# Kernel tuning notes

Hardware: AMD Instinct MI355X
Metric: run time of the kernel (lower is better)

Reference implementation:

```python
import jax, jax.numpy as jnp
import numpy as np

B, S, D, MD = 4, 4096, 1024, 512
SCALE = 0.02  # init scale for weights


def _layernorm(x, g, b, eps=1e-5):
    m = jnp.mean(x, axis=-1, keepdims=True)
    v = jnp.mean((x - m) ** 2, axis=-1, keepdims=True)
    return (x - m) * jax.lax.rsqrt(v + eps) * g + b


def _mem_mlp(h, W0, W1):
    # MemoryMLP depth=2: linear -> gelu -> linear (no biases)
    return jax.nn.gelu(h @ W0) @ W1


def _assoc_scan(gates, inputs):
    # state_t = g_t * state_{t-1} + in_t, over the seq axis (axis=1)
    def step(state, gi):
        g, i = gi
        s = g * state + i
        return s, s
    init = jnp.zeros_like(inputs[:, 0])
    _, out = jax.lax.scan(step, init, (jnp.moveaxis(gates, 1, 0), jnp.moveaxis(inputs, 1, 0)))
    return jnp.moveaxis(out, 1, 0)


def setup_inputs() -> dict:
    key = jax.random.key(0)
    ks = jax.random.split(key, 10)
    return {
        "x": jax.random.normal(ks[0], (B, S, D), jnp.float32),
        "Wd": jax.random.normal(ks[1], (D, MD), jnp.float32) * SCALE,
        "bd": jnp.zeros((MD,), jnp.float32),
        "Wu": jax.random.normal(ks[2], (MD, D), jnp.float32) * SCALE,
        "bu": jnp.zeros((D,), jnp.float32),
        "Wq": jax.random.normal(ks[3], (MD, MD), jnp.float32) * SCALE,
        "bq": jnp.zeros((MD,), jnp.float32),
        "Wk": jax.random.normal(ks[4], (MD, MD), jnp.float32) * SCALE,
        "bk": jnp.zeros((MD,), jnp.float32),
        "Wv": jax.random.normal(ks[5], (MD, MD), jnp.float32) * SCALE,
        "bv": jnp.zeros((MD,), jnp.float32),
        "q_gamma": jnp.ones((MD,), jnp.float32),
        "q_beta": jnp.zeros((MD,), jnp.float32),
        "k_gamma": jnp.ones((MD,), jnp.float32),
        "k_beta": jnp.zeros((MD,), jnp.float32),
        "W0": jax.random.normal(ks[6], (MD, MD), jnp.float32) * SCALE,
        "W1": jax.random.normal(ks[7], (MD, MD), jnp.float32) * SCALE,
        "adaptive_lr": jnp.full((1,), 0.01, jnp.float32),
        "forget_factor": jnp.full((1,), 0.1, jnp.float32),
    }


def reference(x, Wd, bd, Wu, bu, Wq, bq, Wk, bk, Wv, bv,
              q_gamma, q_beta, k_gamma, k_beta, W0, W1,
              adaptive_lr, forget_factor):
    h = x @ Wd + bd                                   # [B,S,MD] down_proj
    q = _layernorm(h @ Wq + bq, q_gamma, q_beta)      # q_norm(to_queries)
    k = _layernorm(h @ Wk + bk, k_gamma, k_beta)      # k_norm(to_keys)
    v = h @ Wv + bv                                   # to_values
    retrieved = _mem_mlp(q, W0, W1)                   # memory read
    pred = _mem_mlp(k, W0, W1)                        # memory store pred
    # per-token surprise: MSE over feature dim
    surprise = jnp.mean((pred - v) ** 2, axis=-1, keepdims=True)  # [B,S,1]
    gate_val = 1.0 - jax.nn.sigmoid(forget_factor)[0]
    gates = jnp.full((B, S, 1), 1.0, jnp.float32) * gate_val
    inputs = adaptive_lr[0] * surprise * v            # surprise-weighted write
    scanned = _assoc_scan(gates, inputs)              # sequential recurrence
    out = (retrieved + scanned) @ Wu + bu             # up_proj
    return out
```

## Files before the change

kernel.cpp:

```cpp
#include <hip/hip_runtime.h>
#include <hip/hip_bf16.h>
#include <math.h>

#define B_    4
#define S_    4096
#define DD    1024
#define MD    512
#define NTOK  16384
#define CHUNK 32
#define NCH   128

typedef unsigned short u16;
typedef unsigned int u32;
typedef __attribute__((ext_vector_type(8))) short short8;
typedef __attribute__((ext_vector_type(4))) float f32x4;
typedef __attribute__((ext_vector_type(4))) unsigned short us4;

__device__ __forceinline__ float bf2f(u16 u) {
    u32 x = ((u32)u) << 16;
    return __builtin_bit_cast(float, x);
}
__device__ __forceinline__ u16 f2bf(float f) {
    u32 x = __builtin_bit_cast(u32, f);
    u32 lsb = (x >> 16) & 1u;
    x += 0x7fffu + lsb;
    return (u16)(x >> 16);
}
__device__ __forceinline__ float gelu_f(float x) {
    float x3 = x * x * x;
    return 0.5f * x * (1.0f + tanhf(0.7978845608028654f * (x + 0.044715f * x3)));
}
__device__ __forceinline__ float gate_from_ff(const float* ff) {
    return 1.0f - 1.0f / (1.0f + expf(-ff[0]));
}

#define GLDS(gp, lp) __builtin_amdgcn_global_load_lds( \
    (const __attribute__((address_space(1))) void*)(gp), \
    (__attribute__((address_space(3))) void*)(lp), 16, 0, 0)

template<int NF, int EPI, int HB, int OUTBF, int SEG>
__global__ __launch_bounds__(256) void gemm_bf16_k(
    const u16* __restrict__ A, const u16* __restrict__ BT,
    const float* __restrict__ bias0, const float* __restrict__ bias1,
    const float* __restrict__ bias2,
    void* __restrict__ out0, void* __restrict__ out1, void* __restrict__ out2,
    int N, int K, int M, int OM)
{
    constexpr int TN = 32 * NF;
    __shared__ __align__(16) u16 Al[2][128 * 32];
    __shared__ __align__(16) u16 Bl[2][TN * 32];
    const int tid = threadIdx.x;
    const int w = tid >> 6, l = tid & 63;
    const int rowBase = blockIdx.y * 128, colBase = blockIdx.x * TN;
    const int wm = (w >> 1) * 64, wn = (w & 1) * 16 * NF;

    const int srow = l >> 2;
    const int skoff = (l & 3) * 8;
    const u16* Ag0 = A + (size_t)(rowBase + w * 16 + srow) * K + skoff;
    const u16* Ag1 = A + (size_t)(rowBase + (w + 4) * 16 + srow) * K + skoff;
    const u16* Bg0 = BT + (size_t)(colBase + w * 16 + srow) * K + skoff;
    const u16* Bg1 = (NF == 4) ? BT + (size_t)(colBase + (w + 4) * 16 + srow) * K + skoff : nullptr;

    f32x4 acc[4][NF];
#pragma unroll
    for (int i = 0; i < 4; ++i)
#pragma unroll
        for (int j = 0; j < NF; ++j) acc[i][j] = (f32x4){0.f, 0.f, 0.f, 0.f};

    const int KT = K >> 5;
    GLDS(Ag0, &Al[0][(w * 16) * 32]);
    GLDS(Ag1, &Al[0][((w + 4) * 16) * 32]);
    GLDS(Bg0, &Bl[0][(w * 16) * 32]);
    if (NF == 4) GLDS(Bg1, &Bl[0][((w + 4) * 16) * 32]);
    __syncthreads();

    const int lr = l & 15;
    const int goff = (l >> 4) * 8;
    int cur = 0;
    for (int kt = 0; kt < KT; ++kt) {
        if (kt + 1 < KT) {
            const size_t ko = (size_t)(kt + 1) << 5;
            GLDS(Ag0 + ko, &Al[cur ^ 1][(w * 16) * 32]);
            GLDS(Ag1 + ko, &Al[cur ^ 1][((w + 4) * 16) * 32]);
            GLDS(Bg0 + ko, &Bl[cur ^ 1][(w * 16) * 32]);
            if (NF == 4) GLDS(Bg1 + ko, &Bl[cur ^ 1][((w + 4) * 16) * 32]);
        }
        short8 af[4], bfr[NF];
#pragma unroll
        for (int m = 0; m < 4; ++m)
            af[m] = *(const short8*)&Al[cur][(wm + m * 16 + lr) * 32 + goff];
#pragma unroll
        for (int n = 0; n < NF; ++n)
            bfr[n] = *(const short8*)&Bl[cur][(wn + n * 16 + lr) * 32 + goff];
#pragma unroll
        for (int m = 0; m < 4; ++m)
#pragma unroll
            for (int n = 0; n < NF; ++n)
                acc[m][n] = __builtin_amdgcn_mfma_f32_16x16x32_bf16(af[m], bfr[n], acc[m][n], 0, 0, 0);
        __syncthreads();
        cur ^= 1;
    }

    const int g4 = (l >> 4) * 4;
    const bool odd = l & 1;
#pragma unroll
    for (int n = 0; n < NF; ++n) {
        const int col = colBase + wn + n * 16 + lr;
        const int seg = SEG ? (col >> 9) : 0;
        const int lcol = SEG ? (col - (seg << 9)) : col;
        const float* bp = (seg == 0) ? bias0 : (seg == 1) ? bias1 : bias2;
        void* outp = (seg == 0) ? out0 : (seg == 1) ? out1 : out2;
        const float bj = HB ? bp[lcol] : 0.0f;
#pragma unroll
        for (int m = 0; m < 4; ++m) {
            const int row0 = rowBase + wm + m * 16 + g4;
            float vq[4];
#pragma unroll
            for (int q = 0; q < 4; ++q) {
                float vv = acc[m][n][q] + bj;
                if (EPI == 1) vv = gelu_f(vv);
                vq[q] = vv;
            }
            if (OUTBF) {
                float pv[4];
#pragma unroll
                for (int q = 0; q < 4; ++q) pv[q] = __shfl_xor(vq[q], 1);
                const int q0 = odd ? 2 : 0;
                u16* ob = (u16*)outp;
#pragma unroll
                for (int j = 0; j < 2; ++j) {
                    const int qq = q0 + j;
                    float lo = odd ? pv[qq] : vq[qq];
                    float hi = odd ? vq[qq] : pv[qq];
                    u32 word = (u32)f2bf(lo) | ((u32)f2bf(hi) << 16);
                    *(u32*)(ob + (size_t)(row0 + qq) * OM + (lcol & ~1)) = word;
                }
            } else {
#pragma unroll
                for (int q = 0; q < 4; ++q)
                    ((float*)outp)[(size_t)(row0 + q) * OM + lcol] = vq[q];
            }
        }
    }
}

__global__ __launch_bounds__(256) void cvt_bf16_k(const float* __restrict__ in,
                                                  u16* __restrict__ out, int n)
{
    size_t i = ((size_t)blockIdx.x * 256 + threadIdx.x) * 8;
    if (i + 8 > (size_t)n) return;
    float4 a = *(const float4*)(in + i);
    float4 b = *(const float4*)(in + i + 4);
    short8 o;
    o[0] = (short)f2bf(a.x); o[1] = (short)f2bf(a.y);
    o[2] = (short)f2bf(a.z); o[3] = (short)f2bf(a.w);
    o[4] = (short)f2bf(b.x); o[5] = (short)f2bf(b.y);
    o[6] = (short)f2bf(b.z); o[7] = (short)f2bf(b.w);
    *(short8*)(out + i) = o;
}

__global__ __launch_bounds__(256) void wtrans_k(const float* __restrict__ W,
                                                u16* __restrict__ WT, int K, int M)
{
    __shared__ float t[32][33];
    const int tx = threadIdx.x, ty = threadIdx.y;
    const int m0 = blockIdx.x * 32, k0 = blockIdx.y * 32;
#pragma unroll
    for (int i = 0; i < 4; ++i)
        t[ty + i * 8][tx] = W[(size_t)(k0 + ty + i * 8) * M + m0 + tx];
    __syncthreads();
#pragma unroll
    for (int i = 0; i < 4; ++i)
        WT[(size_t)(m0 + ty + i * 8) * K + k0 + tx] = f2bf(t[tx][ty + i * 8]);
}

__global__ __launch_bounds__(256) void wtrans5_k(
    const float* __restrict__ Wa, const float* __restrict__ Wb,
    const float* __restrict__ Wc, const float* __restrict__ Wd_,
    const float* __restrict__ We,
    u16* __restrict__ Ta, u16* __restrict__ Tb, u16* __restrict__ Tc,
    u16* __restrict__ Td, u16* __restrict__ Te)
{
    __shared__ float t[32][33];
    const float* W; u16* T;
    switch (blockIdx.z) {
        case 0: W = Wa; T = Ta; break;
        case 1: W = Wb; T = Tb; break;
        case 2: W = Wc; T = Tc; break;
        case 3: W = Wd_; T = Td; break;
        default: W = We; T = Te; break;
    }
    const int tx = threadIdx.x, ty = threadIdx.y;
    const int m0 = blockIdx.x * 32, k0 = blockIdx.y * 32;
#pragma unroll
    for (int i = 0; i < 4; ++i)
        t[ty + i * 8][tx] = W[(size_t)(k0 + ty + i * 8) * 512 + m0 + tx];
    __syncthreads();
#pragma unroll
    for (int i = 0; i < 4; ++i)
        T[(size_t)(m0 + ty + i * 8) * 512 + k0 + tx] = f2bf(t[tx][ty + i * 8]);
}

__global__ __launch_bounds__(256) void ln2_k(u16* __restrict__ X0, u16* __restrict__ X1,
                                             const float* __restrict__ g0, const float* __restrict__ b0,
                                             const float* __restrict__ g1, const float* __restrict__ b1)
{
    const int row = blockIdx.x, tid = threadIdx.x;
    u16* x = (blockIdx.y ? X1 : X0) + (size_t)row * MD;
    const float* g = blockIdx.y ? g1 : g0;
    const float* b = blockIdx.y ? b1 : b0;
    float v0 = bf2f(x[tid]), v1 = bf2f(x[tid + 256]);
    float s = v0 + v1, q = v0 * v0 + v1 * v1;
#pragma unroll
    for (int off = 32; off > 0; off >>= 1) {
        s += __shfl_down(s, off);
        q += __shfl_down(q, off);
    }
    __shared__ float redS[4], redQ[4];
    __shared__ float s_mean, s_rstd;
    const int lane = tid & 63, w = tid >> 6;
    if (lane == 0) { redS[w] = s; redQ[w] = q; }
    __syncthreads();
    if (tid == 0) {
        float S = redS[0] + redS[1] + redS[2] + redS[3];
        float Q = redQ[0] + redQ[1] + redQ[2] + redQ[3];
        float m = S * (1.f / 512.f);
        float var = Q * (1.f / 512.f) - m * m;
        s_mean = m; s_rstd = rsqrtf(var + 1e-5f);
    }
    __syncthreads();
    const float m = s_mean, rs = s_rstd;
    x[tid]       = f2bf((v0 - m) * rs * g[tid]       + b[tid]);
    x[tid + 256] = f2bf((v1 - m) * rs * g[tid + 256] + b[tid + 256]);
}

__global__ __launch_bounds__(256) void surprise_k(const u16* __restrict__ pred,
                                                  const u16* __restrict__ v,
                                                  const float* __restrict__ lr_p,
                                                  float* __restrict__ coef)
{
    const int row = blockIdx.x, tid = threadIdx.x;
    const u16* pp = pred + (size_t)row * MD;
    const u16* vp = v + (size_t)row * MD;
    float d0 = bf2f(pp[tid]) - bf2f(vp[tid]);
    float d1 = bf2f(pp[tid + 256]) - bf2f(vp[tid + 256]);
    float q = d0 * d0 + d1 * d1;
#pragma unroll
    for (int off = 32; off > 0; off >>= 1) q += __shfl_down(q, off);
    __shared__ float redQ[4];
    const int lane = tid & 63, w = tid >> 6;
    if (lane == 0) redQ[w] = q;
    __syncthreads();
    if (tid == 0) {
        float Q = redQ[0] + redQ[1] + redQ[2] + redQ[3];
        coef[row] = lr_p[0] * (Q * (1.f / 512.f));
    }
}

__global__ __launch_bounds__(256) void scan1_k(u16* __restrict__ io,
                                               const float* __restrict__ coef,
                                               const float* __restrict__ ff,
                                               float* __restrict__ carry)
{
    const int idx = blockIdx.x * blockDim.x + threadIdx.x;
    const int d4 = (idx & 127) * 4;
    const int c = (idx >> 7) & (NCH - 1);
    const int b = idx >> 14;
    const float g = gate_from_ff(ff);
    const int tok0 = b * S_ + c * CHUNK;
    u16* p = io + (size_t)tok0 * MD + d4;
    const float* cf = coef + tok0;
    float s0 = 0.f, s1 = 0.f, s2 = 0.f, s3 = 0.f;
#pragma unroll 4
    for (int t = 0; t < CHUNK; ++t) {
        us4 vv = *(const us4*)(p + (size_t)t * MD);
        const float ct = cf[t];
        s0 = fmaf(g, s0, ct * bf2f(vv.x));
        s1 = fmaf(g, s1, ct * bf2f(vv.y));
        s2 = fmaf(g, s2, ct * bf2f(vv.z));
        s3 = fmaf(g, s3, ct * bf2f(vv.w));
        us4 ov = { f2bf(s0), f2bf(s1), f2bf(s2), f2bf(s3) };
        *(us4*)(p + (size_t)t * MD) = ov;
    }
    float4 cw = { s0, s1, s2, s3 };
    *(float4*)(carry + ((size_t)b * NCH + c) * MD + d4) = cw;
}

__global__ __launch_bounds__(256) void scan2_k(const float* __restrict__ carry,
                                               const float* __restrict__ ff,
                                               float* __restrict__ Sin)
{
    const int idx = blockIdx.x * blockDim.x + threadIdx.x;
    const int d = idx & (MD - 1);
    const int b = idx >> 9;
    const float g = gate_from_ff(ff);
    const float gL = powf(g, (float)CHUNK);
    float p = 0.f;
    for (int c = 0; c < NCH; ++c) {
        Sin[((size_t)b * NCH + c) * MD + d] = p;
        p = carry[((size_t)b * NCH + c) * MD + d] + gL * p;
    }
}

__global__ __launch_bounds__(256) void scan3_k(const u16* __restrict__ loc,
                                               const float* __restrict__ Sin,
                                               const u16* __restrict__ retr,
                                               const float* __restrict__ ff,
                                               u16* __restrict__ fin)
{
    const size_t idx = (size_t)blockIdx.x * blockDim.x + threadIdx.x;
    const int d4 = (int)(idx & 127) * 4;
    const int t = (int)((idx >> 7) & (S_ - 1));
    const int b = (int)(idx >> 19);
    const int c = t >> 5, tl = t & (CHUNK - 1);
    const float g = gate_from_ff(ff);
    const float f = exp2f((float)(tl + 1) * log2f(g));
    const size_t row = (size_t)(b * S_ + t) * MD + d4;
    us4 lv = *(const us4*)(loc + row);
    us4 rv = *(const us4*)(retr + row);
    float4 sv = *(const float4*)(Sin + ((size_t)b * NCH + c) * MD + d4);
    us4 ov;
    ov.x = f2bf(bf2f(lv.x) + f * sv.x + bf2f(rv.x));
    ov.y = f2bf(bf2f(lv.y) + f * sv.y + bf2f(rv.y));
    ov.z = f2bf(bf2f(lv.z) + f * sv.z + bf2f(rv.z));
    ov.w = f2bf(bf2f(lv.w) + f * sv.w + bf2f(rv.w));
    *(us4*)(fin + row) = ov;
}

extern "C" void kernel_launch(void* const* d_in, const int* in_sizes, int n_in,
                              void* d_out, int out_size, void* d_ws, size_t ws_size,
                              hipStream_t stream) {
    const float* x   = (const float*)d_in[0];
    const float* Wd  = (const float*)d_in[1];
    const float* bd  = (const float*)d_in[2];
    const float* Wu  = (const float*)d_in[3];
    const float* bu  = (const float*)d_in[4];
    const float* Wq  = (const float*)d_in[5];
    const float* bq  = (const float*)d_in[6];
    const float* Wk  = (const float*)d_in[7];
    const float* bk  = (const float*)d_in[8];
    const float* Wv  = (const float*)d_in[9];
    const float* bv  = (const float*)d_in[10];
    const float* qg  = (const float*)d_in[11];
    const float* qb  = (const float*)d_in[12];
    const float* kg  = (const float*)d_in[13];
    const float* kb  = (const float*)d_in[14];
    const float* W0  = (const float*)d_in[15];
    const float* W1  = (const float*)d_in[16];
    const float* lr  = (const float*)d_in[17];
    const float* ff  = (const float*)d_in[18];
    float* out = (float*)d_out;

    u16* wdT   = (u16*)d_ws;
    u16* wqkvT = wdT + 512 * 1024;
    u16* w0T   = wqkvT + 1536 * 512;
    u16* w1T   = w0T + 512 * 512;
    u16* wuT   = w1T + 512 * 512;
    u16* xb    = wuT + 1024 * 512;
    u16* hb    = xb + (size_t)NTOK * DD;
    u16* b1    = hb + (size_t)NTOK * MD;
    u16* b2    = b1 + (size_t)NTOK * MD;
    u16* VB    = b2 + (size_t)NTOK * MD;
    float* coef  = (float*)(VB + (size_t)NTOK * MD);
    float* carry = coef + NTOK;
    float* Sin   = carry + (size_t)B_ * NCH * MD;

    dim3 blk(256);
    dim3 t32(32, 8);

    cvt_bf16_k<<<(NTOK * DD) / (256 * 8), blk, 0, stream>>>(x, xb, NTOK * DD);
    wtrans_k<<<dim3(16, 32), t32, 0, stream>>>(Wd, wdT, 1024, 512);
    wtrans5_k<<<dim3(16, 16, 5), t32, 0, stream>>>(Wq, Wk, Wv, W0, W1,
        wqkvT, wqkvT + 512 * 512, wqkvT + 2 * 512 * 512, w0T, w1T);
    wtrans_k<<<dim3(32, 16), t32, 0, stream>>>(Wu, wuT, 512, 1024);

    gemm_bf16_k<2, 0, 1, 1, 0><<<dim3(8, 128), blk, 0, stream>>>(
        xb, wdT, bd, bd, bd, hb, hb, hb, NTOK, 1024, 512, 512);
    gemm_bf16_k<4, 0, 1, 1, 1><<<dim3(12, 128), blk, 0, stream>>>(
        hb, wqkvT, bq, bk, bv, b1, b2, VB, NTOK, 512, 1536, 512);
    ln2_k<<<dim3(NTOK, 2), blk, 0, stream>>>(b1, b2, qg, qb, kg, kb);
    gemm_bf16_k<4, 1, 0, 1, 0><<<dim3(4, 256), blk, 0, stream>>>(
        b1, w0T, nullptr, nullptr, nullptr, xb, xb, xb, 2 * NTOK, 512, 512, 512);
    gemm_bf16_k<4, 0, 0, 1, 0><<<dim3(4, 256), blk, 0, stream>>>(
        xb, w1T, nullptr, nullptr, nullptr, b1, b1, b1, 2 * NTOK, 512, 512, 512);
    surprise_k<<<NTOK, blk, 0, stream>>>(b2, VB, lr, coef);
    scan1_k<<<(B_ * NCH * (MD / 4)) / 256, blk, 0, stream>>>(VB, coef, ff, carry);
    scan2_k<<<(B_ * MD) / 256, blk, 0, stream>>>(carry, ff, Sin);
    scan3_k<<<(NTOK * (MD / 4)) / 256, blk, 0, stream>>>(VB, Sin, b1, ff, b2);
    gemm_bf16_k<4, 0, 1, 0, 0><<<dim3(8, 128), blk, 0, stream>>>(
        b2, wuT, bu, bu, bu, out, out, out, NTOK, 512, 1024, 1024);
}
```

Measured before the change: 360.7 us.

## Use 128x128 GEMM tiles, XCD-aware block swizzle, and LDS-staged coalesced bf16 stores

```diff
diff --git a/kernel.cpp b/kernel.cpp
--- a/kernel.cpp
+++ b/kernel.cpp
@@ -38,40 +38,46 @@
     (const __attribute__((address_space(1))) void*)(gp), \
     (__attribute__((address_space(3))) void*)(lp), 16, 0, 0)
 
-template<int NF, int EPI, int HB, int OUTBF, int SEG>
+template<int EPI, int HB, int OUTBF, int SEG>
 __global__ __launch_bounds__(256) void gemm_bf16_k(
     const u16* __restrict__ A, const u16* __restrict__ BT,
     const float* __restrict__ bias0, const float* __restrict__ bias1,
     const float* __restrict__ bias2,
     void* __restrict__ out0, void* __restrict__ out1, void* __restrict__ out2,
-    int N, int K, int M, int OM)
-{
-    constexpr int TN = 32 * NF;
+    int K, int gx, int OM)
+{
     __shared__ __align__(16) u16 Al[2][128 * 32];
-    __shared__ __align__(16) u16 Bl[2][TN * 32];
+    __shared__ __align__(16) u16 Bl[2][128 * 32];
     const int tid = threadIdx.x;
     const int w = tid >> 6, l = tid & 63;
-    const int rowBase = blockIdx.y * 128, colBase = blockIdx.x * TN;
-    const int wm = (w >> 1) * 64, wn = (w & 1) * 16 * NF;
+
+    const int nwg = gridDim.x;
+    const int cpx = nwg >> 3;
+    const int o = blockIdx.x;
+    const int swz = (o & 7) * cpx + (o >> 3);
+    const int bx = swz % gx, by = swz / gx;
+
+    const int rowBase = by * 128, colBase = bx * 128;
+    const int wm = (w >> 1) * 64, wn = (w & 1) * 64;
 
     const int srow = l >> 2;
     const int skoff = (l & 3) * 8;
     const u16* Ag0 = A + (size_t)(rowBase + w * 16 + srow) * K + skoff;
     const u16* Ag1 = A + (size_t)(rowBase + (w + 4) * 16 + srow) * K + skoff;
     const u16* Bg0 = BT + (size_t)(colBase + w * 16 + srow) * K + skoff;
-    const u16* Bg1 = (NF == 4) ? BT + (size_t)(colBase + (w + 4) * 16 + srow) * K + skoff : nullptr;
-
-    f32x4 acc[4][NF];
+    const u16* Bg1 = BT + (size_t)(colBase + (w + 4) * 16 + srow) * K + skoff;
+
+    f32x4 acc[4][4];
 #pragma unroll
     for (int i = 0; i < 4; ++i)
 #pragma unroll
-        for (int j = 0; j < NF; ++j) acc[i][j] = (f32x4){0.f, 0.f, 0.f, 0.f};
+        for (int j = 0; j < 4; ++j) acc[i][j] = (f32x4){0.f, 0.f, 0.f, 0.f};
 
     const int KT = K >> 5;
     GLDS(Ag0, &Al[0][(w * 16) * 32]);
     GLDS(Ag1, &Al[0][((w + 4) * 16) * 32]);
     GLDS(Bg0, &Bl[0][(w * 16) * 32]);
-    if (NF == 4) GLDS(Bg1, &Bl[0][((w + 4) * 16) * 32]);
+    GLDS(Bg1, &Bl[0][((w + 4) * 16) * 32]);
     __syncthreads();
 
     const int lr = l & 15;
@@ -83,62 +89,88 @@
             GLDS(Ag0 + ko, &Al[cur ^ 1][(w * 16) * 32]);
             GLDS(Ag1 + ko, &Al[cur ^ 1][((w + 4) * 16) * 32]);
             GLDS(Bg0 + ko, &Bl[cur ^ 1][(w * 16) * 32]);
-            if (NF == 4) GLDS(Bg1 + ko, &Bl[cur ^ 1][((w + 4) * 16) * 32]);
+            GLDS(Bg1 + ko, &Bl[cur ^ 1][((w + 4) * 16) * 32]);
         }
-        short8 af[4], bfr[NF];
+        short8 af[4], bfr[4];
 #pragma unroll
         for (int m = 0; m < 4; ++m)
             af[m] = *(const short8*)&Al[cur][(wm + m * 16 + lr) * 32 + goff];
 #pragma unroll
-        for (int n = 0; n < NF; ++n)
+        for (int n = 0; n < 4; ++n)
             bfr[n] = *(const short8*)&Bl[cur][(wn + n * 16 + lr) * 32 + goff];
 #pragma unroll
         for (int m = 0; m < 4; ++m)
 #pragma unroll
-            for (int n = 0; n < NF; ++n)
+            for (int n = 0; n < 4; ++n)
                 acc[m][n] = __builtin_amdgcn_mfma_f32_16x16x32_bf16(af[m], bfr[n], acc[m][n], 0, 0, 0);
         __syncthreads();
         cur ^= 1;
     }
 
     const int g4 = (l >> 4) * 4;
-    const bool odd = l & 1;
-#pragma unroll
-    for (int n = 0; n < NF; ++n) {
-        const int col = colBase + wn + n * 16 + lr;
-        const int seg = SEG ? (col >> 9) : 0;
-        const int lcol = SEG ? (col - (seg << 9)) : col;
-        const float* bp = (seg == 0) ? bias0 : (seg == 1) ? bias1 : bias2;
-        void* outp = (seg == 0) ? out0 : (seg == 1) ? out1 : out2;
-        const float bj = HB ? bp[lcol] : 0.0f;
+    const int wcol0 = colBase + wn;
+    const int seg = SEG ? (wcol0 >> 9) : 0;
+    const int lcol0 = SEG ? (wcol0 - (seg << 9)) : wcol0;
+    const float* bp = (seg == 0) ? bias0 : (seg == 1) ? bias1 : bias2;
+    void* outp = (seg == 0) ? out0 : (seg == 1) ? out1 : out2;
+
+    if (OUTBF) {
+        u16* scr = &Al[0][0] + w * 1024;
+        u16* ob = (u16*)outp;
+        const bool odd = l & 1;
+        const int lrp = lr & ~1;
 #pragma unroll
         for (int m = 0; m < 4; ++m) {
-            const int row0 = rowBase + wm + m * 16 + g4;
-            float vq[4];
-#pragma unroll
-            for (int q = 0; q < 4; ++q) {
-                float vv = acc[m][n][q] + bj;
-                if (EPI == 1) vv = gelu_f(vv);
-                vq[q] = vv;
+            const int baseRow = rowBase + wm + m * 16;
+            float vq[4][4];
+#pragma unroll
+            for (int n = 0; n < 4; ++n) {
+                const float bj = HB ? bp[lcol0 + n * 16 + lr] : 0.0f;
+#pragma unroll
+                for (int q = 0; q < 4; ++q) {
+                    float vv = acc[m][n][q] + bj;
+                    if (EPI == 1) vv = gelu_f(vv);
+                    vq[n][q] = vv;
+                }
             }
-            if (OUTBF) {
+#pragma unroll
+            for (int n = 0; n < 4; ++n) {
                 float pv[4];
 #pragma unroll
-                for (int q = 0; q < 4; ++q) pv[q] = __shfl_xor(vq[q], 1);
+                for (int q = 0; q < 4; ++q) pv[q] = __shfl_xor(vq[n][q], 1);
                 const int q0 = odd ? 2 : 0;
-                u16* ob = (u16*)outp;
 #pragma unroll
                 for (int j = 0; j < 2; ++j) {
                     const int qq = q0 + j;
-                    float lo = odd ? pv[qq] : vq[qq];
-                    float hi = odd ? vq[qq] : pv[qq];
+                    float lo = odd ? pv[qq] : vq[n][qq];
+                    float hi = odd ? vq[n][qq] : pv[qq];
                     u32 word = (u32)f2bf(lo) | ((u32)f2bf(hi) << 16);
-                    *(u32*)(ob + (size_t)(row0 + qq) * OM + (lcol & ~1)) = word;
+                    *(u32*)&scr[(g4 + qq) * 64 + n * 16 + lrp] = word;
                 }
-            } else {
-#pragma unroll
-                for (int q = 0; q < 4; ++q)
-                    ((float*)outp)[(size_t)(row0 + q) * OM + lcol] = vq[q];
+            }
+            asm volatile("s_waitcnt lgkmcnt(0)" ::: "memory");
+            __builtin_amdgcn_sched_barrier(0);
+            short8 r0 = *(const short8*)&scr[(l >> 3) * 64 + (l & 7) * 8];
+            short8 r1 = *(const short8*)&scr[((l >> 3) + 8) * 64 + (l & 7) * 8];
+            const size_t gaddr = (size_t)(baseRow + (l >> 3)) * OM + lcol0 + (l & 7) * 8;
+            *(short8*)(ob + gaddr) = r0;
+            *(short8*)(ob + gaddr + (size_t)8 * OM) = r1;
+            __builtin_amdgcn_sched_barrier(0);
+        }
+    } else {
+#pragma unroll
+        for (int n = 0; n < 4; ++n) {
+            const int col = lcol0 + n * 16 + lr;
+            const float bj = HB ? bp[col] : 0.0f;
+#pragma unroll
+            for (int m = 0; m < 4; ++m) {
+                const int row0 = rowBase + wm + m * 16 + g4;
+#pragma unroll
+                for (int q = 0; q < 4; ++q) {
+                    float vv = acc[m][n][q] + bj;
+                    if (EPI == 1) vv = gelu_f(vv);
+                    ((float*)outp)[(size_t)(row0 + q) * OM + col] = vv;
+                }
             }
         }
     }
@@ -374,19 +406,19 @@
         wqkvT, wqkvT + 512 * 512, wqkvT + 2 * 512 * 512, w0T, w1T);
     wtrans_k<<<dim3(32, 16), t32, 0, stream>>>(Wu, wuT, 512, 1024);
 
-    gemm_bf16_k<2, 0, 1, 1, 0><<<dim3(8, 128), blk, 0, stream>>>(
-        xb, wdT, bd, bd, bd, hb, hb, hb, NTOK, 1024, 512, 512);
-    gemm_bf16_k<4, 0, 1, 1, 1><<<dim3(12, 128), blk, 0, stream>>>(
-        hb, wqkvT, bq, bk, bv, b1, b2, VB, NTOK, 512, 1536, 512);
+    gemm_bf16_k<0, 1, 1, 0><<<dim3(512), blk, 0, stream>>>(
+        xb, wdT, bd, bd, bd, hb, hb, hb, 1024, 4, 512);
+    gemm_bf16_k<0, 1, 1, 1><<<dim3(1536), blk, 0, stream>>>(
+        hb, wqkvT, bq, bk, bv, b1, b2, VB, 512, 12, 512);
     ln2_k<<<dim3(NTOK, 2), blk, 0, stream>>>(b1, b2, qg, qb, kg, kb);
-    gemm_bf16_k<4, 1, 0, 1, 0><<<dim3(4, 256), blk, 0, stream>>>(
-        b1, w0T, nullptr, nullptr, nullptr, xb, xb, xb, 2 * NTOK, 512, 512, 512);
-    gemm_bf16_k<4, 0, 0, 1, 0><<<dim3(4, 256), blk, 0, stream>>>(
-        xb, w1T, nullptr, nullptr, nullptr, b1, b1, b1, 2 * NTOK, 512, 512, 512);
+    gemm_bf16_k<1, 0, 1, 0><<<dim3(1024), blk, 0, stream>>>(
+        b1, w0T, nullptr, nullptr, nullptr, xb, xb, xb, 512, 4, 512);
+    gemm_bf16_k<0, 0, 1, 0><<<dim3(1024), blk, 0, stream>>>(
+        xb, w1T, nullptr, nullptr, nullptr, b1, b1, b1, 512, 4, 512);
     surprise_k<<<NTOK, blk, 0, stream>>>(b2, VB, lr, coef);
     scan1_k<<<(B_ * NCH * (MD / 4)) / 256, blk, 0, stream>>>(VB, coef, ff, carry);
     scan2_k<<<(B_ * MD) / 256, blk, 0, stream>>>(carry, ff, Sin);
     scan3_k<<<(NTOK * (MD / 4)) / 256, blk, 0, stream>>>(VB, Sin, b1, ff, b2);
-    gemm_bf16_k<4, 0, 1, 0, 0><<<dim3(8, 128), blk, 0, stream>>>(
-        b2, wuT, bu, bu, bu, out, out, out, NTOK, 512, 1024, 1024);
-}
+    gemm_bf16_k<0, 1, 0, 0><<<dim3(1024), blk, 0, stream>>>(
+        b2, wuT, bu, bu, bu, out, out, out, 512, 8, 1024);
+}
```

Measured after the change: 330.6 us. -8.3%, faster.
